# Performance work log

Hardware: AMD Instinct MI355X
Metric: run time of the kernel (lower is better)

Reference implementation:

```python
import jax, jax.numpy as jnp
import numpy as np

N = 50000      # nodes
F = 256        # num_features
H = 128        # hidden_size
R = 16         # num_relations
E = 800000     # edges
C = 7          # num_classes
NB = 30        # num_bases (hard-coded in module)


def setup_inputs() -> dict:
    key = jax.random.key(0)
    ks = jax.random.split(key, 16)
    g = lambda k, shape, fan_in: jax.random.normal(k, shape, jnp.float32) / np.float32(np.sqrt(fan_in))
    inp = {
        "x": jax.random.normal(ks[0], (N, F), jnp.float32),
        "edge_index": jax.random.randint(ks[1], (2, E), 0, N),
        "edge_norm": jax.random.uniform(ks[2], (E,), jnp.float32),
        "edge_type": jax.random.randint(ks[3], (E,), 0, R),
        "seq_lengths": jax.random.randint(ks[4], (16,), 1, 100),
        "umask": jnp.ones((16, 110), jnp.float32),
        "nodal_attn": 0,
        "avec": 0,
        # RGCNConv (basis decomposition)
        "basis": g(ks[5], (NB, F, H), F),
        "comp": g(ks[6], (R, NB), NB),
        "root1": g(ks[7], (F, H), F),
        "bias1": jnp.zeros((H,), jnp.float32),
        # GraphConv
        "w_rel": g(ks[8], (H, H), H),
        "w_root": g(ks[9], (H, H), H),
        "bias2": jnp.zeros((H,), jnp.float32),
        # classification head
        "lin_w": g(ks[10], (F + H, H), F + H),
        "lin_b": jnp.zeros((H,), jnp.float32),
        "fc_w": g(ks[11], (H, C), H),
        "fc_b": jnp.zeros((C,), jnp.float32),
    }
    return inp


def reference(x, edge_index, edge_norm, edge_type, seq_lengths, umask,
              nodal_attn, avec, basis, comp, root1, bias1,
              w_rel, w_root, bias2, lin_w, lin_b, fc_w, fc_b):
    src, dst = edge_index[0], edge_index[1]

    # ---- RGCNConv: basis-decomposed relational conv, mean aggr per relation ----
    W = jnp.einsum('rb,bio->rio', comp, basis)          # [R,F,H]
    xW = jnp.einsum('ni,rio->nro', x, W)                # [N,R,H]
    msgs = xW[src, edge_type]                           # [E,H]
    seg = dst * R + edge_type                           # (dst, relation) segment id
    cnt = jax.ops.segment_sum(jnp.ones((E,), jnp.float32), seg, num_segments=N * R)
    inv = 1.0 / jnp.maximum(cnt, 1.0)
    agg1 = jax.ops.segment_sum(msgs * inv[seg][:, None], dst, num_segments=N)
    out1 = agg1 + x @ root1 + bias1                     # [N,H]

    # ---- GraphConv: sum aggr + root transform ----
    agg2 = jax.ops.segment_sum(out1[src], dst, num_segments=N)  # [N,H]
    out2 = agg2 @ w_rel + bias2 + out1 @ w_root         # [N,H]

    # ---- classification head (nodal_attn=False path; dropout is identity in eval) ----
    emotions = jnp.concatenate([x, out2], axis=-1)      # [N,F+H]
    hidden = jax.nn.relu(emotions @ lin_w + lin_b)      # [N,H]
    logits = hidden @ fc_w + fc_b                       # [N,C]
    return jax.nn.log_softmax(logits, axis=1)
```

## Files before the change

### kernel.cpp

```cpp
#include <hip/hip_runtime.h>
#include <hip/hip_bf16.h>
#include <stdint.h>

#define NN 50000
#define FF 256
#define HH 128
#define RR 16
#define EE 800000
#define CC 7
#define NB_ 30

typedef __attribute__((ext_vector_type(8))) short short8;
typedef __attribute__((ext_vector_type(4))) float f32x4;

__device__ __forceinline__ float bf2f(unsigned short u){
  union { unsigned int i; float f; } x; x.i = ((unsigned int)u) << 16; return x.f;
}
__device__ __forceinline__ unsigned short f2bf(float f){
  union { unsigned int i; float f; } x; x.f = f;
  unsigned int r = x.i + 0x7fffu + ((x.i >> 16) & 1u);
  return (unsigned short)(r >> 16);
}

__device__ __forceinline__ void gld16(const unsigned short* g, unsigned short* l){
  __builtin_amdgcn_global_load_lds(
      (const __attribute__((address_space(1))) unsigned int*)g,
      (__attribute__((address_space(3))) unsigned int*)l, 16, 0, 0);
}

template<bool BIAS, bool RELU, bool G1>
__global__ __launch_bounds__(256) void gemm_bt(
    const unsigned short* __restrict__ A0, int ldA0,
    const unsigned short* __restrict__ A1, int ldA1, int kSplit,
    const unsigned short* __restrict__ Bt,
    unsigned short* __restrict__ Cout, int ldC,
    const float* __restrict__ bias,
    int M, int K,
    unsigned short* __restrict__ out1, const float* __restrict__ bias1)
{
  __shared__ unsigned short Al[2][128*64];
  __shared__ unsigned short Bl[2][128*64];
  const int tid  = threadIdx.x;
  const int lane = tid & 63;
  const int wid  = tid >> 6;
  const int wr   = wid >> 1, wc = wid & 1;

  int bm, bn;
  if (G1){
    int orig = blockIdx.x;
    int xcd  = orig & 7, sub = orig >> 3;
    int cidx = (xcd < 7 ? xcd*831 : 7*831) + sub;
    int p    = cidx / 136;
    int wres = cidx - p*136;
    int ph   = min(8, 391 - p*8);
    bn = wres / ph;
    bm = p*8 + wres % ph;
  } else {
    bm = blockIdx.x; bn = blockIdx.y;
  }

  const int nkt = K >> 6;

  auto STAGE = [&](int kt, int pb){
    int c0 = kt*64;
    const unsigned short* Asrc = A0; int lda = ldA0;
    if (c0 >= kSplit){ Asrc = A1; lda = ldA1; c0 -= kSplit; }
    const unsigned short* arow = Asrc + (size_t)(bm*128 + wid*32 + (lane>>3))*lda + c0 + (lane&7)*8;
    const unsigned short* brow = Bt   + (size_t)(bn*128 + wid*32 + (lane>>3))*K  + kt*64 + (lane&7)*8;
    #pragma unroll
    for (int i=0;i<4;i++){
      gld16(arow + (size_t)i*8*lda, &Al[pb][(wid*32 + i*8)*64]);
      gld16(brow + (size_t)i*8*K,   &Bl[pb][(wid*32 + i*8)*64]);
    }
  };

  f32x4 acc[4][4];
  #pragma unroll
  for (int m=0;m<4;m++)
    #pragma unroll
    for (int n=0;n<4;n++) acc[m][n] = (f32x4){0.f,0.f,0.f,0.f};

  STAGE(0, 0);
  __syncthreads();

  int pb = 0;
  for (int kt=0; kt<nkt; ++kt){
    if (kt+1 < nkt) STAGE(kt+1, pb^1);
    #pragma unroll
    for (int ks=0; ks<2; ++ks){
      short8 a[4], b[4];
      #pragma unroll
      for (int m=0;m<4;m++)
        a[m] = *(const short8*)&Al[pb][(wr*64 + m*16 + (lane&15))*64 + ks*32 + (lane>>4)*8];
      #pragma unroll
      for (int n=0;n<4;n++)
        b[n] = *(const short8*)&Bl[pb][(wc*64 + n*16 + (lane&15))*64 + ks*32 + (lane>>4)*8];
      #pragma unroll
      for (int m=0;m<4;m++)
        #pragma unroll
        for (int n=0;n<4;n++)
          acc[m][n] = __builtin_amdgcn_mfma_f32_16x16x32_bf16(b[n], a[m], acc[m][n], 0, 0, 0);
    }
    __syncthreads();
    pb ^= 1;
  }

  #pragma unroll
  for (int m=0;m<4;m++){
    int row = bm*128 + wr*64 + m*16 + (lane&15);
    if (row < M){
      #pragma unroll
      for (int n=0;n<4;n++){
        int colr = wc*64 + n*16 + ((lane>>4)<<2);
        float v0 = acc[m][n][0], v1 = acc[m][n][1], v2 = acc[m][n][2], v3 = acc[m][n][3];
        if (G1){
          if (bn == 16){
            v0 += bias1[colr]; v1 += bias1[colr+1]; v2 += bias1[colr+2]; v3 += bias1[colr+3];
            unsigned int lo = (unsigned int)f2bf(v0) | ((unsigned int)f2bf(v1) << 16);
            unsigned int hi = (unsigned int)f2bf(v2) | ((unsigned int)f2bf(v3) << 16);
            *(uint2*)&out1[(size_t)row*HH + colr] = make_uint2(lo, hi);
          } else {
            unsigned int lo = (unsigned int)f2bf(v0) | ((unsigned int)f2bf(v1) << 16);
            unsigned int hi = (unsigned int)f2bf(v2) | ((unsigned int)f2bf(v3) << 16);
            *(uint2*)&Cout[(size_t)row*2048 + bn*128 + colr] = make_uint2(lo, hi);
          }
        } else {
          int col = bn*128 + colr;
          if (BIAS){ v0 += bias[col]; v1 += bias[col+1]; v2 += bias[col+2]; v3 += bias[col+3]; }
          if (RELU){ v0 = fmaxf(v0,0.f); v1 = fmaxf(v1,0.f); v2 = fmaxf(v2,0.f); v3 = fmaxf(v3,0.f); }
          unsigned int lo = (unsigned int)f2bf(v0) | ((unsigned int)f2bf(v1) << 16);
          unsigned int hi = (unsigned int)f2bf(v2) | ((unsigned int)f2bf(v3) << 16);
          *(uint2*)&Cout[(size_t)row*ldC + col] = make_uint2(lo, hi);
        }
      }
    }
  }
}

__global__ void k_cvt(const float* __restrict__ in, unsigned short* __restrict__ out, int n4){
  int i = blockIdx.x*256 + threadIdx.x;
  if (i >= n4) return;
  float4 v = ((const float4*)in)[i];
  union { unsigned short u[4]; uint2 q; } t;
  t.u[0]=f2bf(v.x); t.u[1]=f2bf(v.y); t.u[2]=f2bf(v.z); t.u[3]=f2bf(v.w);
  ((uint2*)out)[i] = t.q;
}

__global__ __launch_bounds__(256) void k_build_wt(const float* __restrict__ comp,
                                                  const float* __restrict__ basis,
                                                  unsigned short* __restrict__ WT){
  __shared__ float sm[16][129];
  __shared__ float cmp[NB_];
  int r = blockIdx.x >> 4, i0 = (blockIdx.x & 15)*16;
  int o = threadIdx.x & 127, ih = threadIdx.x >> 7;
  if (threadIdx.x < NB_) cmp[threadIdx.x] = comp[r*NB_ + threadIdx.x];
  __syncthreads();
  #pragma unroll
  for (int step=0; step<8; ++step){
    int i = i0 + step*2 + ih;
    float s = 0.f;
    #pragma unroll 6
    for (int b=0;b<NB_;b++) s += cmp[b]*basis[((size_t)b*FF + i)*HH + o];
    sm[step*2+ih][o] = s;
  }
  __syncthreads();
  #pragma unroll
  for (int w=0;w<8;w++){
    int o2 = w*16 + (threadIdx.x>>4);
    int ii = threadIdx.x & 15;
    WT[((size_t)(r*128 + o2))*FF + i0 + ii] = f2bf(sm[ii][o2]);
  }
}

__global__ void k_transpose_cat(const float* __restrict__ in0, int k0,
                                const float* __restrict__ in1, int k1,
                                unsigned short* __restrict__ outT){
  int K = k0 + k1;
  int idx = blockIdx.x*256 + threadIdx.x;
  if (idx >= 128*K) return;
  int o = idx / K, k = idx % K;
  float v = (k < k0) ? in0[(size_t)k*HH + o] : in1[(size_t)(k-k0)*HH + o];
  outT[idx] = f2bf(v);
}

__global__ void k_count(const int* __restrict__ dstv, int* __restrict__ counts){
  int e = blockIdx.x*256 + threadIdx.x;
  if (e >= EE) return;
  atomicAdd(&counts[dstv[e]], 1);
}

__global__ __launch_bounds__(256) void k_scan1(const int* __restrict__ counts,
                                               int* __restrict__ row_ptr,
                                               int* __restrict__ blocksum){
  __shared__ int wsum[4];
  int g = blockIdx.x*256 + threadIdx.x;
  int lane = threadIdx.x & 63, wv = threadIdx.x >> 6;
  int v = (g < NN) ? counts[g] : 0;
  int s = v;
  #pragma unroll
  for (int off=1; off<64; off<<=1){ int t = __shfl_up(s, off, 64); if (lane>=off) s += t; }
  if (lane==63) wsum[wv] = s;
  __syncthreads();
  int wo = 0;
  #pragma unroll
  for (int i=0;i<4;i++) if (i < wv) wo += wsum[i];
  int incl = s + wo;
  if (g < NN) row_ptr[g] = incl - v;
  if (threadIdx.x == 255) blocksum[blockIdx.x] = incl;
}
__global__ __launch_bounds__(256) void k_scan2(int* __restrict__ blocksum, int nb){
  __shared__ int wsum[4];
  int t = threadIdx.x, lane = t & 63, wv = t >> 6;
  int v = (t < nb) ? blocksum[t] : 0;
  int s = v;
  #pragma unroll
  for (int off=1; off<64; off<<=1){ int u = __shfl_up(s, off, 64); if (lane>=off) s += u; }
  if (lane==63) wsum[wv] = s;
  __syncthreads();
  int wo = 0;
  #pragma unroll
  for (int i=0;i<4;i++) if (i < wv) wo += wsum[i];
  if (t < nb) blocksum[t] = s + wo - v;
}
__global__ __launch_bounds__(256) void k_scan3(int* __restrict__ row_ptr,
                                               const int* __restrict__ blocksum){
  int g = blockIdx.x*256 + threadIdx.x;
  if (g < NN) row_ptr[g] += blocksum[blockIdx.x];
  if (g == 0) row_ptr[NN] = EE;
}

__global__ void k_fill(const int* __restrict__ srcv, const int* __restrict__ dstv,
                       const int* __restrict__ etv, const int* __restrict__ row_ptr,
                       int* __restrict__ cursor, int* __restrict__ packed){
  int e = blockIdx.x*256 + threadIdx.x;
  if (e >= EE) return;
  int d = dstv[e];
  int p = atomicAdd(&cursor[d], 1);
  packed[row_ptr[d] + p] = (srcv[e] & 0xffff) | (etv[e] << 16);
}

__global__ __launch_bounds__(256) void k_agg1(const int* __restrict__ row_ptr,
                                              const int* __restrict__ packed,
                                              const unsigned int* __restrict__ xWu,
                                              unsigned int* __restrict__ out1u){
  __shared__ int   cnt[4][RR];
  __shared__ float inv[4][RR];
  const int lane = threadIdx.x & 63;
  const int wv   = threadIdx.x >> 6;
  const int node = blockIdx.x*4 + wv;
  if (lane < RR) cnt[wv][lane] = 0;
  __syncthreads();
  const int b0 = row_ptr[node], b1 = row_ptr[node+1];
  for (int j=b0+lane; j<b1; j+=64) atomicAdd(&cnt[wv][(packed[j]>>16)&15], 1);
  __syncthreads();
  if (lane < RR) inv[wv][lane] = 1.0f / fmaxf((float)cnt[wv][lane], 1.0f);
  __syncthreads();

  float a0=0.f, a1=0.f;
  int j = b0;
  for (; j+8 <= b1; j+=8){
    int pv[8]; unsigned int vv[8];
    #pragma unroll
    for (int q=0;q<8;q++) pv[q] = packed[j+q];
    #pragma unroll
    for (int q=0;q<8;q++)
      vv[q] = xWu[((size_t)(((pv[q]&0xffff)<<4)|((pv[q]>>16)&15)) << 6) + lane];
    #pragma unroll
    for (int q=0;q<8;q++){
      float f = inv[wv][(pv[q]>>16)&15];
      a0 += bf2f((unsigned short)vv[q])*f;
      a1 += bf2f((unsigned short)(vv[q]>>16))*f;
    }
  }
  for (; j+4 <= b1; j+=4){
    int pv[4]; unsigned int vv[4];
    #pragma unroll
    for (int q=0;q<4;q++) pv[q] = packed[j+q];
    #pragma unroll
    for (int q=0;q<4;q++)
      vv[q] = xWu[((size_t)(((pv[q]&0xffff)<<4)|((pv[q]>>16)&15)) << 6) + lane];
    #pragma unroll
    for (int q=0;q<4;q++){
      float f = inv[wv][(pv[q]>>16)&15];
      a0 += bf2f((unsigned short)vv[q])*f;
      a1 += bf2f((unsigned short)(vv[q]>>16))*f;
    }
  }
  for (; j<b1; ++j){
    int p = packed[j];
    unsigned int v = xWu[((size_t)(((p&0xffff)<<4)|((p>>16)&15)) << 6) + lane];
    float f = inv[wv][(p>>16)&15];
    a0 += bf2f((unsigned short)v)*f;
    a1 += bf2f((unsigned short)(v>>16))*f;
  }
  size_t o = (size_t)node*64 + lane;
  unsigned int cur = out1u[o];
  float r0 = bf2f((unsigned short)cur)       + a0;
  float r1 = bf2f((unsigned short)(cur>>16)) + a1;
  out1u[o] = (unsigned int)f2bf(r0) | ((unsigned int)f2bf(r1) << 16);
}

__global__ __launch_bounds__(256) void k_agg2(const int* __restrict__ row_ptr,
                                              const int* __restrict__ packed,
                                              const unsigned int* __restrict__ out1u,
                                              unsigned int* __restrict__ agg2u){
  const int lane = threadIdx.x & 63;
  const int wv   = threadIdx.x >> 6;
  const int node = blockIdx.x*4 + wv;
  const int b0 = row_ptr[node], b1 = row_ptr[node+1];
  float a0=0.f, a1=0.f;
  int j = b0;
  for (; j+8 <= b1; j+=8){
    unsigned int vv[8];
    #pragma unroll
    for (int q=0;q<8;q++)
      vv[q] = out1u[(size_t)(packed[j+q]&0xffff)*64 + lane];
    #pragma unroll
    for (int q=0;q<8;q++){
      a0 += bf2f((unsigned short)vv[q]);
      a1 += bf2f((unsigned short)(vv[q]>>16));
    }
  }
  for (; j+4 <= b1; j+=4){
    unsigned int vv[4];
    #pragma unroll
    for (int q=0;q<4;q++)
      vv[q] = out1u[(size_t)(packed[j+q]&0xffff)*64 + lane];
    #pragma unroll
    for (int q=0;q<4;q++){
      a0 += bf2f((unsigned short)vv[q]);
      a1 += bf2f((unsigned short)(vv[q]>>16));
    }
  }
  for (; j<b1; ++j){
    unsigned int v = out1u[(size_t)(packed[j]&0xffff)*64 + lane];
    a0 += bf2f((unsigned short)v);
    a1 += bf2f((unsigned short)(v>>16));
  }
  agg2u[(size_t)node*64 + lane] = (unsigned int)f2bf(a0) | ((unsigned int)f2bf(a1) << 16);
}

__global__ __launch_bounds__(256) void k_head(const unsigned short* __restrict__ hidden,
                                              const float* __restrict__ fc_w,
                                              const float* __restrict__ fc_b,
                                              float* __restrict__ out){
  int node = blockIdx.x*4 + (threadIdx.x >> 6);
  int lane = threadIdx.x & 63;
  if (node >= NN) return;
  float h0 = bf2f(hidden[(size_t)node*128 + lane*2]);
  float h1 = bf2f(hidden[(size_t)node*128 + lane*2 + 1]);
  float lg[CC];
  #pragma unroll
  for (int c=0;c<CC;c++){
    float p = h0*fc_w[(lane*2)*CC + c] + h1*fc_w[(lane*2+1)*CC + c];
    #pragma unroll
    for (int off=32; off; off>>=1) p += __shfl_down(p, off, 64);
    lg[c] = p;
  }
  if (lane == 0){
    float l[CC]; float m = -1e30f;
    #pragma unroll
    for (int c=0;c<CC;c++){ l[c] = lg[c] + fc_b[c]; m = fmaxf(m, l[c]); }
    float s = 0.f;
    #pragma unroll
    for (int c=0;c<CC;c++) s += expf(l[c]-m);
    float lse = logf(s);
    #pragma unroll
    for (int c=0;c<CC;c++) out[(size_t)node*CC + c] = l[c] - m - lse;
  }
}

extern "C" void kernel_launch(void* const* d_in, const int* in_sizes, int n_in,
                              void* d_out, int out_size, void* d_ws, size_t ws_size,
                              hipStream_t stream)
{
  const float* x      = (const float*)d_in[0];
  const int*   eidx   = (const int*)d_in[1];
  const int*   etype  = (const int*)d_in[3];
  const float* basis  = (const float*)d_in[8];
  const float* comp   = (const float*)d_in[9];
  const float* root1  = (const float*)d_in[10];
  const float* bias1  = (const float*)d_in[11];
  const float* w_rel  = (const float*)d_in[12];
  const float* w_root = (const float*)d_in[13];
  const float* bias2  = (const float*)d_in[14];
  const float* lin_w  = (const float*)d_in[15];
  const float* lin_b  = (const float*)d_in[16];
  const float* fc_w   = (const float*)d_in[17];
  const float* fc_b   = (const float*)d_in[18];
  const int* srcv = eidx;
  const int* dstv = eidx + EE;

  char* w = (char*)d_ws;
  unsigned short* x_bf    = (unsigned short*)(w + 0);
  unsigned short* xW      = (unsigned short*)(w + 25624576);
  unsigned short* hidden  = (unsigned short*)(w + 25624576);
  unsigned short* out2_bf = (unsigned short*)(w + 25624576 + 12812288);
  unsigned short* agg2_bf = (unsigned short*)(w + 25624576 + 25624576);
  unsigned short* WT      = (unsigned short*)(w + 230424576);
  unsigned short* rootT   = (unsigned short*)(w + 231473152);
  unsigned short* W2T     = (unsigned short*)(w + 231538688);
  unsigned short* linT    = (unsigned short*)(w + 231604224);
  unsigned short* out1_bf = (unsigned short*)(w + 231702528);
  int*            counts  = (int*)(w + 244514816);
  int*            row_ptr = (int*)(w + 244715008);
  int*            cursor  = (int*)(w + 244915200);
  int*            packed  = (int*)(w + 245115392);
  int*            blocksum= (int*)(w + 248315392);
  (void)rootT;

  hipMemsetAsync(counts, 0, NN*4, stream);
  hipMemsetAsync(cursor, 0, NN*4, stream);

  k_cvt<<<12500, 256, 0, stream>>>(x, x_bf, NN*FF/4);
  k_build_wt<<<256, 256, 0, stream>>>(comp, basis, WT);
  k_transpose_cat<<<128, 256, 0, stream>>>(root1, 256, nullptr, 0, rootT);
  k_transpose_cat<<<128, 256, 0, stream>>>(w_rel, 128, w_root, 128, W2T);
  k_transpose_cat<<<192, 256, 0, stream>>>(lin_w, 384, nullptr, 0, linT);

  k_count<<<3125, 256, 0, stream>>>(dstv, counts);
  k_scan1<<<196, 256, 0, stream>>>(counts, row_ptr, blocksum);
  k_scan2<<<1, 256, 0, stream>>>(blocksum, 196);
  k_scan3<<<196, 256, 0, stream>>>(row_ptr, blocksum);
  k_fill<<<3125, 256, 0, stream>>>(srcv, dstv, etype, row_ptr, cursor, packed);

  gemm_bt<false,false,true><<<6647, 256, 0, stream>>>(
      x_bf, FF, nullptr, 0, 1<<30, WT, xW, 2048, nullptr, NN, FF, out1_bf, bias1);
  k_agg1<<<12500, 256, 0, stream>>>(row_ptr, packed, (const unsigned int*)xW, (unsigned int*)out1_bf);
  k_agg2<<<12500, 256, 0, stream>>>(row_ptr, packed, (const unsigned int*)out1_bf, (unsigned int*)agg2_bf);
  {
    dim3 g(391, 1);
    gemm_bt<true,false,false><<<g, 256, 0, stream>>>(
        agg2_bf, HH, out1_bf, HH, HH, W2T, out2_bf, HH, bias2, NN, 2*HH, nullptr, nullptr);
  }
  {
    dim3 g(391, 1);
    gemm_bt<true,true,false><<<g, 256, 0, stream>>>(
        x_bf, FF, out2_bf, HH, FF, linT, hidden, HH, lin_b, NN, FF+HH, nullptr, nullptr);
  }
  k_head<<<12500, 256, 0, stream>>>(hidden, fc_w, fc_b, (float*)d_out);
}
```

Baseline: 440.7 us.

## Fuse classification head into final GEMM and swizzle single-buffered LDS tiles

The fc head and log-softmax now run inside the last GEMM's epilogue. ReLU'd hidden tiles are written to shared memory and each wave reduces 32 rows, so the separate k_head launch and the hidden-tensor round trip through global memory go away. The GEMM also drops double buffering for a single XOR-swizzled LDS buffer, halving shared memory to cut bank conflicts and raise occupancy. The cost is losing the load/compute overlap in every GEMM, including the large first one.

Measured after the change: 440.7 us. Within noise of the previous version (+0.0%).

```diff
diff --git a/kernel.cpp b/kernel.cpp
--- a/kernel.cpp
+++ b/kernel.cpp
@@ -28,7 +28,7 @@
       (__attribute__((address_space(3))) unsigned int*)l, 16, 0, 0);
 }
 
-template<bool BIAS, bool RELU, bool G1>
+template<bool BIAS, bool RELU, bool G1, bool FHEAD>
 __global__ __launch_bounds__(256) void gemm_bt(
     const unsigned short* __restrict__ A0, int ldA0,
     const unsigned short* __restrict__ A1, int ldA1, int kSplit,
@@ -36,10 +36,13 @@
     unsigned short* __restrict__ Cout, int ldC,
     const float* __restrict__ bias,
     int M, int K,
-    unsigned short* __restrict__ out1, const float* __restrict__ bias1)
+    unsigned short* __restrict__ out1, const float* __restrict__ bias1,
+    const float* __restrict__ fc_w, const float* __restrict__ fc_b,
+    float* __restrict__ fout)
 {
-  __shared__ unsigned short Al[2][128*64];
-  __shared__ unsigned short Bl[2][128*64];
+  __shared__ unsigned short smem[2][128*64];
+  unsigned short* Al = smem[0];
+  unsigned short* Bl = smem[1];
   const int tid  = threadIdx.x;
   const int lane = tid & 63;
   const int wid  = tid >> 6;
@@ -60,41 +63,37 @@
   }
 
   const int nkt = K >> 6;
-
-  auto STAGE = [&](int kt, int pb){
+  const int r8  = lane >> 3;
+  const int sw  = ((lane & 7) ^ r8) * 8;
+
+  f32x4 acc[4][4];
+  #pragma unroll
+  for (int m=0;m<4;m++)
+    #pragma unroll
+    for (int n=0;n<4;n++) acc[m][n] = (f32x4){0.f,0.f,0.f,0.f};
+
+  for (int kt=0; kt<nkt; ++kt){
     int c0 = kt*64;
     const unsigned short* Asrc = A0; int lda = ldA0;
     if (c0 >= kSplit){ Asrc = A1; lda = ldA1; c0 -= kSplit; }
-    const unsigned short* arow = Asrc + (size_t)(bm*128 + wid*32 + (lane>>3))*lda + c0 + (lane&7)*8;
-    const unsigned short* brow = Bt   + (size_t)(bn*128 + wid*32 + (lane>>3))*K  + kt*64 + (lane&7)*8;
+    const unsigned short* arow = Asrc + (size_t)(bm*128 + wid*32 + r8)*lda + c0 + sw;
+    const unsigned short* brow = Bt   + (size_t)(bn*128 + wid*32 + r8)*K  + kt*64 + sw;
     #pragma unroll
     for (int i=0;i<4;i++){
-      gld16(arow + (size_t)i*8*lda, &Al[pb][(wid*32 + i*8)*64]);
-      gld16(brow + (size_t)i*8*K,   &Bl[pb][(wid*32 + i*8)*64]);
-    }
-  };
-
-  f32x4 acc[4][4];
-  #pragma unroll
-  for (int m=0;m<4;m++)
-    #pragma unroll
-    for (int n=0;n<4;n++) acc[m][n] = (f32x4){0.f,0.f,0.f,0.f};
-
-  STAGE(0, 0);
-  __syncthreads();
-
-  int pb = 0;
-  for (int kt=0; kt<nkt; ++kt){
-    if (kt+1 < nkt) STAGE(kt+1, pb^1);
+      gld16(arow + (size_t)(i*8)*lda, &Al[(wid*32 + i*8)*64]);
+      gld16(brow + (size_t)(i*8)*K,   &Bl[(wid*32 + i*8)*64]);
+    }
+    __syncthreads();
     #pragma unroll
     for (int ks=0; ks<2; ++ks){
+      const int slot = ((ks<<2) + (lane>>4)) ^ (lane&7);
       short8 a[4], b[4];
       #pragma unroll
       for (int m=0;m<4;m++)
-        a[m] = *(const short8*)&Al[pb][(wr*64 + m*16 + (lane&15))*64 + ks*32 + (lane>>4)*8];
+        a[m] = *(const short8*)&Al[(wr*64 + m*16 + (lane&15))*64 + slot*8];
       #pragma unroll
       for (int n=0;n<4;n++)
-        b[n] = *(const short8*)&Bl[pb][(wc*64 + n*16 + (lane&15))*64 + ks*32 + (lane>>4)*8];
+        b[n] = *(const short8*)&Bl[(wc*64 + n*16 + (lane&15))*64 + slot*8];
       #pragma unroll
       for (int m=0;m<4;m++)
         #pragma unroll
@@ -102,7 +101,61 @@
           acc[m][n] = __builtin_amdgcn_mfma_f32_16x16x32_bf16(b[n], a[m], acc[m][n], 0, 0, 0);
     }
     __syncthreads();
-    pb ^= 1;
+  }
+
+  if (FHEAD){
+    unsigned int* Hu = (unsigned int*)smem;
+    #pragma unroll
+    for (int m=0;m<4;m++){
+      int row = wr*64 + m*16 + (lane&15);
+      #pragma unroll
+      for (int n=0;n<4;n++){
+        int cbase = wc*64 + n*16 + ((lane>>4)<<2);
+        float v0 = acc[m][n][0] + bias[cbase];
+        float v1 = acc[m][n][1] + bias[cbase+1];
+        float v2 = acc[m][n][2] + bias[cbase+2];
+        float v3 = acc[m][n][3] + bias[cbase+3];
+        v0 = fmaxf(v0,0.f); v1 = fmaxf(v1,0.f); v2 = fmaxf(v2,0.f); v3 = fmaxf(v3,0.f);
+        int cp = (cbase>>1) ^ ((row&7)<<1);
+        Hu[row*64 + cp    ] = (unsigned int)f2bf(v0) | ((unsigned int)f2bf(v1) << 16);
+        Hu[row*64 + cp + 1] = (unsigned int)f2bf(v2) | ((unsigned int)f2bf(v3) << 16);
+      }
+    }
+    __syncthreads();
+    float w0[CC], w1[CC];
+    #pragma unroll
+    for (int c=0;c<CC;c++){
+      w0[c] = fc_w[(lane*2)*CC + c];
+      w1[c] = fc_w[(lane*2+1)*CC + c];
+    }
+    for (int i=0;i<32;i++){
+      int r = wid*32 + i;
+      int node = bm*128 + r;
+      if (node >= NN) break;
+      unsigned int h = Hu[r*64 + (((lane>>1) ^ (r&7))<<1) + (lane&1)];
+      float h0 = bf2f((unsigned short)h);
+      float h1 = bf2f((unsigned short)(h>>16));
+      float lg[CC];
+      #pragma unroll
+      for (int c=0;c<CC;c++){
+        float p = h0*w0[c] + h1*w1[c];
+        #pragma unroll
+        for (int off=32; off; off>>=1) p += __shfl_down(p, off, 64);
+        lg[c] = p;
+      }
+      if (lane == 0){
+        float l[CC]; float mx = -1e30f;
+        #pragma unroll
+        for (int c=0;c<CC;c++){ l[c] = lg[c] + fc_b[c]; mx = fmaxf(mx, l[c]); }
+        float s = 0.f;
+        #pragma unroll
+        for (int c=0;c<CC;c++) s += expf(l[c]-mx);
+        float lse = logf(s);
+        #pragma unroll
+        for (int c=0;c<CC;c++) fout[(size_t)node*CC + c] = l[c] - mx - lse;
+      }
+    }
+    return;
   }
 
   #pragma unroll
@@ -340,36 +393,6 @@
   agg2u[(size_t)node*64 + lane] = (unsigned int)f2bf(a0) | ((unsigned int)f2bf(a1) << 16);
 }
 
-__global__ __launch_bounds__(256) void k_head(const unsigned short* __restrict__ hidden,
-                                              const float* __restrict__ fc_w,
-                                              const float* __restrict__ fc_b,
-                                              float* __restrict__ out){
-  int node = blockIdx.x*4 + (threadIdx.x >> 6);
-  int lane = threadIdx.x & 63;
-  if (node >= NN) return;
-  float h0 = bf2f(hidden[(size_t)node*128 + lane*2]);
-  float h1 = bf2f(hidden[(size_t)node*128 + lane*2 + 1]);
-  float lg[CC];
-  #pragma unroll
-  for (int c=0;c<CC;c++){
-    float p = h0*fc_w[(lane*2)*CC + c] + h1*fc_w[(lane*2+1)*CC + c];
-    #pragma unroll
-    for (int off=32; off; off>>=1) p += __shfl_down(p, off, 64);
-    lg[c] = p;
-  }
-  if (lane == 0){
-    float l[CC]; float m = -1e30f;
-    #pragma unroll
-    for (int c=0;c<CC;c++){ l[c] = lg[c] + fc_b[c]; m = fmaxf(m, l[c]); }
-    float s = 0.f;
-    #pragma unroll
-    for (int c=0;c<CC;c++) s += expf(l[c]-m);
-    float lse = logf(s);
-    #pragma unroll
-    for (int c=0;c<CC;c++) out[(size_t)node*CC + c] = l[c] - m - lse;
-  }
-}
-
 extern "C" void kernel_launch(void* const* d_in, const int* in_sizes, int n_in,
                               void* d_out, int out_size, void* d_ws, size_t ws_size,
                               hipStream_t stream)
@@ -394,7 +417,6 @@
   char* w = (char*)d_ws;
   unsigned short* x_bf    = (unsigned short*)(w + 0);
   unsigned short* xW      = (unsigned short*)(w + 25624576);
-  unsigned short* hidden  = (unsigned short*)(w + 25624576);
   unsigned short* out2_bf = (unsigned short*)(w + 25624576 + 12812288);
   unsigned short* agg2_bf = (unsigned short*)(w + 25624576 + 25624576);
   unsigned short* WT      = (unsigned short*)(w + 230424576);
@@ -424,19 +446,21 @@
   k_scan3<<<196, 256, 0, stream>>>(row_ptr, blocksum);
   k_fill<<<3125, 256, 0, stream>>>(srcv, dstv, etype, row_ptr, cursor, packed);
 
-  gemm_bt<false,false,true><<<6647, 256, 0, stream>>>(
-      x_bf, FF, nullptr, 0, 1<<30, WT, xW, 2048, nullptr, NN, FF, out1_bf, bias1);
+  gemm_bt<false,false,true,false><<<6647, 256, 0, stream>>>(
+      x_bf, FF, nullptr, 0, 1<<30, WT, xW, 2048, nullptr, NN, FF,
+      out1_bf, bias1, nullptr, nullptr, nullptr);
   k_agg1<<<12500, 256, 0, stream>>>(row_ptr, packed, (const unsigned int*)xW, (unsigned int*)out1_bf);
   k_agg2<<<12500, 256, 0, stream>>>(row_ptr, packed, (const unsigned int*)out1_bf, (unsigned int*)agg2_bf);
   {
     dim3 g(391, 1);
-    gemm_bt<true,false,false><<<g, 256, 0, stream>>>(
-        agg2_bf, HH, out1_bf, HH, HH, W2T, out2_bf, HH, bias2, NN, 2*HH, nullptr, nullptr);
+    gemm_bt<true,false,false,false><<<g, 256, 0, stream>>>(
+        agg2_bf, HH, out1_bf, HH, HH, W2T, out2_bf, HH, bias2, NN, 2*HH,
+        nullptr, nullptr, nullptr, nullptr, nullptr);
   }
   {
     dim3 g(391, 1);
-    gemm_bt<true,true,false><<<g, 256, 0, stream>>>(
-        x_bf, FF, out2_bf, HH, FF, linT, hidden, HH, lin_b, NN, FF+HH, nullptr, nullptr);
-  }
-  k_head<<<12500, 256, 0, stream>>>(hidden, fc_w, fc_b, (float*)d_out);
-}
+    gemm_bt<true,true,false,true><<<g, 256, 0, stream>>>(
+        x_bf, FF, out2_bf, HH, FF, linT, nullptr, HH, lin_b, NN, FF+HH,
+        nullptr, nullptr, fc_w, fc_b, (float*)d_out);
+  }
+}
```
